# Performance work log

Measured on AMD Instinct MI355X. Metric: run time of the kernel, lower is better.

The kernel has to match this reference:

```python
import jax, jax.numpy as jnp
import numpy as np
import math

G = 128          # graphs per batch
N_PER = 512      # nodes per graph (equal-size, contiguous layout)
N = G * N_PER    # 65536 nodes
DEG = 16
E = N * DEG      # 1,048,576 edges
IN_C, HID, OUT_C = 100, 128, 2
RATIO = 0.8
EPS = 1e-5

K1 = int(math.ceil(RATIO * N_PER))  # 410
K2 = int(math.ceil(RATIO * K1))     # 328
K3 = int(math.ceil(RATIO * K2))     # 263


def gcn_conv(x, src, dst, emask, W, b):
    # GCNConv: linear, symmetric deg^-1/2 norm with self-loops, scatter-add
    xl = x @ W
    n = x.shape[0]
    w = emask.astype(x.dtype)
    deg = jnp.ones((n,), x.dtype).at[dst].add(w)      # +1 from self loop
    dinv = jax.lax.rsqrt(deg)
    coef = dinv[src] * dinv[dst] * w                  # [E]
    out = jnp.zeros_like(xl).at[dst].add(coef[:, None] * xl[src])
    out = out + (dinv * dinv)[:, None] * xl           # self-loop messages
    return out + b


def batch_norm(x, gamma, beta):
    # BatchNorm1d over node dim (training-mode batch statistics)
    mu = x.mean(0)
    var = x.var(0)
    return (x - mu) * jax.lax.rsqrt(var + EPS) * gamma + beta


def topk_pool(x, src, dst, emask, att, g, n, k):
    # TopKPooling: score = tanh(x@att/||att||), keep top-k per graph, gate features,
    # drop edges touching removed nodes (via validity mask).
    score = jnp.tanh((x @ att) / jnp.linalg.norm(att))
    _, idx = jax.lax.top_k(score.reshape(g, n), k)           # [g,k] local ids
    kept = (idx + (jnp.arange(g) * n)[:, None]).reshape(-1)   # global ids
    new_x = x[kept] * score[kept][:, None]
    old2new = jnp.full((g * n,), -1, jnp.int32).at[kept].set(
        jnp.arange(g * k, dtype=jnp.int32))
    s2, d2 = old2new[src], old2new[dst]
    valid = emask & (s2 >= 0) & (d2 >= 0)
    return new_x, jnp.maximum(s2, 0), jnp.maximum(d2, 0), valid


def readout(x, g, k):
    # [global_max_pool, global_mean_pool] over each graph's k nodes
    xr = x.reshape(g, k, -1)
    return jnp.concatenate([xr.max(1), xr.mean(1)], axis=1)   # [g, 2C]


def setup_inputs() -> dict:
    key = jax.random.key(0)
    ks = jax.random.split(key, 16)
    x = jax.random.normal(ks[0], (N, IN_C), jnp.float32)
    # within-graph random edges, then offset by graph id
    e_per = E // G
    local = jax.random.randint(ks[1], (2, G, e_per), 0, N_PER)
    edge_index = (local + (jnp.arange(G) * N_PER)[None, :, None]).reshape(2, E).astype(jnp.int32)
    batch = jnp.repeat(jnp.arange(G, dtype=jnp.int32), N_PER)

    def w(k, fi, fo):
        return jax.random.normal(k, (fi, fo), jnp.float32) * (1.0 / np.sqrt(fi))

    z = lambda c: jnp.zeros((c,), jnp.float32)
    o = lambda c: jnp.ones((c,), jnp.float32)
    return {
        'x': x, 'edge_index': edge_index, 'batch': batch,
        'Wp': w(ks[2], IN_C, 128), 'bp': z(128),
        'W1': w(ks[3], 128, HID), 'b1': z(HID), 'g1': o(HID), 'be1': z(HID),
        'att1': jax.random.normal(ks[4], (HID,), jnp.float32),
        'W2': w(ks[5], HID, HID), 'b2': z(HID), 'g2': o(HID), 'be2': z(HID),
        'att2': jax.random.normal(ks[6], (HID,), jnp.float32),
        'W3': w(ks[7], HID, HID), 'b3': z(HID), 'g3': o(HID), 'be3': z(HID),
        'att3': jax.random.normal(ks[8], (HID,), jnp.float32),
        'Wl1': w(ks[9], 2 * HID, HID), 'bl1': z(HID),
        'Wl2': w(ks[10], HID, OUT_C), 'bl2': z(OUT_C),
    }


def reference(x, edge_index, batch, Wp, bp, W1, b1, g1, be1, att1,
              W2, b2, g2, be2, att2, W3, b3, g3, be3, att3,
              Wl1, bl1, Wl2, bl2):
    src, dst = edge_index[0], edge_index[1]
    emask = jnp.ones((E,), bool)
    h = jax.nn.relu(x @ Wp + bp)

    h = jax.nn.relu(batch_norm(gcn_conv(h, src, dst, emask, W1, b1), g1, be1))
    h, src, dst, emask = topk_pool(h, src, dst, emask, att1, G, N_PER, K1)
    x1 = readout(h, G, K1)

    h = jax.nn.relu(batch_norm(gcn_conv(h, src, dst, emask, W2, b2), g2, be2))
    h, src, dst, emask = topk_pool(h, src, dst, emask, att2, G, K1, K2)
    x2 = readout(h, G, K2)

    h = jax.nn.relu(batch_norm(gcn_conv(h, src, dst, emask, W3, b3), g3, be3))
    h, src, dst, emask = topk_pool(h, src, dst, emask, att3, G, K2, K3)
    x3 = readout(h, G, K3)

    s = x1 + x2 + x3                       # [G, 2*HID]
    s = jax.nn.relu(s @ Wl1 + bl1)
    return s @ Wl2 + bl2                   # [G, OUT_C]
```

## Files before the change

### kernel.cpp

```cpp
#include <hip/hip_runtime.h>
#include <math.h>

#define G     128
#define NPER  512
#define NTOT  65536
#define E_TOT 1048576
#define EPG   8192
#define INC   100
#define HID   128
#define KP1   410
#define KP2   328
#define KP3   263

__global__ void init_kernel(short* __restrict__ cmap, float* __restrict__ sread,
                            float* __restrict__ bnpart) {
    int t = blockIdx.x * 256 + threadIdx.x;
    if (t < NTOT) cmap[t] = (short)(t & (NPER - 1));
    if (t < G * 256) { sread[t] = 0.f; bnpart[t] = 0.f; }
}

__global__ __launch_bounds__(512, 2) void csr_build0(
    const int* __restrict__ src, const int* __restrict__ dst,
    unsigned short* __restrict__ csr_g, int* __restrict__ rowptr_g)
{
    __shared__ int cnt_s[NPER];
    __shared__ int rowptr_s[NPER + 1];
    __shared__ int wo_s[NPER];
    __shared__ int chunksum_s[9];

    const int g = blockIdx.x, tid = threadIdx.x, lane = tid & 63, wv = tid >> 6;
    const int ebase = g * EPG, obase = g * NPER;

    cnt_s[tid] = 0;
    __syncthreads();
    for (int e = tid; e < EPG; e += 512)
        atomicAdd(&cnt_s[dst[ebase + e] - obase], 1);
    __syncthreads();

    int v = cnt_s[tid], x = v;
#pragma unroll
    for (int d = 1; d < 64; d <<= 1) {
        int y = __shfl_up(x, d);
        if (lane >= d) x += y;
    }
    if (lane == 63) chunksum_s[wv] = x;
    __syncthreads();
    if (tid == 0) {
        int acc = 0;
#pragma unroll
        for (int k = 0; k < 8; ++k) { int t = chunksum_s[k]; chunksum_s[k] = acc; acc += t; }
    }
    __syncthreads();
    int excl = x - v + chunksum_s[wv];
    rowptr_s[tid] = excl; wo_s[tid] = excl;
    if (tid == 511) rowptr_s[512] = excl + v;
    __syncthreads();

    for (int i = tid; i <= NPER; i += 512) rowptr_g[g * 513 + i] = rowptr_s[i];
    for (int e = tid; e < EPG; e += 512) {
        int sl = src[ebase + e] - obase, dl = dst[ebase + e] - obase;
        int pos = atomicAdd(&wo_s[dl], 1);
        csr_g[g * EPG + pos] = (unsigned short)sl;
    }
}

template<int K, bool RELU>
__global__ __launch_bounds__(256, 2) void gemm_kernel(
    const float* __restrict__ A, const float* __restrict__ W,
    const float* __restrict__ bias, float* __restrict__ out, int M)
{
    constexpr int KC = 32;
    __shared__ float Ws[KC][128];
    __shared__ float As[KC][132];
    const int tid  = threadIdx.x;
    const int row0 = blockIdx.x * 128;
    const int r0 = (tid >> 4) * 8;
    const int c0 = (tid & 15) * 8;

    float acc[8][8];
#pragma unroll
    for (int i = 0; i < 8; ++i)
#pragma unroll
        for (int j = 0; j < 8; ++j) acc[i][j] = 0.f;

    for (int k0 = 0; k0 < K; k0 += KC) {
        const int kc  = (K - k0 < KC) ? (K - k0) : KC;
        const int nf4 = kc >> 2;

        for (int i = tid; i < kc * 32; i += 256) {
            int kk = i >> 5, c4 = i & 31;
            *((float4*)&Ws[kk][0] + c4) =
                *((const float4*)(W + (size_t)(k0 + kk) * 128) + c4);
        }
        for (int i = tid; i < nf4 * 128; i += 256) {
            int row = i / nf4, f4 = i - row * nf4;
            float4 v = *(const float4*)(A + (size_t)(row0 + row) * K + k0 + f4 * 4);
            As[f4 * 4 + 0][row] = v.x;
            As[f4 * 4 + 1][row] = v.y;
            As[f4 * 4 + 2][row] = v.z;
            As[f4 * 4 + 3][row] = v.w;
        }
        __syncthreads();

        for (int kk = 0; kk < kc; ++kk) {
            float4 b0 = *(const float4*)&Ws[kk][c0];
            float4 b1 = *(const float4*)&Ws[kk][c0 + 4];
            float4 a0 = *(const float4*)&As[kk][r0];
            float4 a1 = *(const float4*)&As[kk][r0 + 4];
            float a[8] = {a0.x, a0.y, a0.z, a0.w, a1.x, a1.y, a1.z, a1.w};
            float b[8] = {b0.x, b0.y, b0.z, b0.w, b1.x, b1.y, b1.z, b1.w};
#pragma unroll
            for (int i = 0; i < 8; ++i)
#pragma unroll
                for (int j = 0; j < 8; ++j)
                    acc[i][j] += a[i] * b[j];
        }
        __syncthreads();
    }

#pragma unroll
    for (int i = 0; i < 8; ++i) {
        int row = row0 + r0 + i;
        float o[8];
#pragma unroll
        for (int j = 0; j < 8; ++j) {
            float v = acc[i][j];
            if (RELU) v = fmaxf(v + bias[c0 + j], 0.f);
            o[j] = v;
        }
        float* po = out + (size_t)row * 128 + c0;
        *(float4*)po       = make_float4(o[0], o[1], o[2], o[3]);
        *(float4*)(po + 4) = make_float4(o[4], o[5], o[6], o[7]);
    }
}

template<int NCUR>
__global__ __launch_bounds__(256, 4) void gather_kernel(
    const float* __restrict__ xs, const unsigned short* __restrict__ csr_g,
    const int* __restrict__ rowptr_g, const float* __restrict__ bvec,
    float* __restrict__ out, float* __restrict__ bnpart)
{
    constexpr int CHUNK = (NCUR + 7) / 8;
    constexpr int CSRCAP = 2560;
    __shared__ int   rowptr_s[NCUR + 1];
    __shared__ float dinv_s[NCUR];
    __shared__ unsigned short csr_s[CSRCAP];
    __shared__ float red_s[512];

    const int g = blockIdx.x, s = blockIdx.y;
    const int tid = threadIdx.x, lane = tid & 63, w = tid >> 6;
    const int nb = g * NCUR;
    const int d0 = s * CHUNK;
    const int d1 = (d0 + CHUNK < NCUR) ? d0 + CHUNK : NCUR;

    const int* rp = rowptr_g + g * 513;
    for (int i = tid; i <= NCUR; i += 256) rowptr_s[i] = rp[i];
    __syncthreads();
    for (int i = tid; i < NCUR; i += 256)
        dinv_s[i] = rsqrtf((float)(rowptr_s[i + 1] - rowptr_s[i] + 1));

    const int base = rowptr_s[d0];
    int nume = rowptr_s[d1] - base;
    if (nume > CSRCAP) nume = CSRCAP;
    const unsigned short* cg = csr_g + g * EPG + base;
    for (int i = tid; i < nume; i += 256) csr_s[i] = cg[i];
    __syncthreads();

    const float2* x2 = (const float2*)xs;
    float2* o2p = (float2*)out;
    const float2 b2 = ((const float2*)bvec)[lane];
    float2 sum = make_float2(0.f, 0.f), sq = make_float2(0.f, 0.f);

    for (int d = d0 + w; d < d1; d += 4) {
        const int beg = rowptr_s[d] - base, end = rowptr_s[d + 1] - base;
        const float dv = dinv_s[d];
        float2 xv = x2[(size_t)(nb + d) * 64 + lane];
        float2 acc = make_float2(dv * xv.x, dv * xv.y);
#pragma unroll 4
        for (int i = beg; i < end; ++i) {
            int sl = csr_s[i];
            float ws_ = dinv_s[sl];
            float2 v = x2[(size_t)(nb + sl) * 64 + lane];
            acc.x += ws_ * v.x; acc.y += ws_ * v.y;
        }
        float2 o = make_float2(b2.x + dv * acc.x, b2.y + dv * acc.y);
        o2p[(size_t)(nb + d) * 64 + lane] = o;
        sum.x += o.x; sum.y += o.y;
        sq.x  += o.x * o.x; sq.y += o.y * o.y;
    }

    float2* red2 = (float2*)red_s;
    red2[tid] = sum; __syncthreads();
    if (tid < 64) {
        float2 a = red2[tid], b_ = red2[tid + 64],
               c = red2[tid + 128], d_ = red2[tid + 192];
        atomicAdd(&bnpart[g * 256 + 2 * tid],     a.x + b_.x + c.x + d_.x);
        atomicAdd(&bnpart[g * 256 + 2 * tid + 1], a.y + b_.y + c.y + d_.y);
    }
    __syncthreads();
    red2[tid] = sq; __syncthreads();
    if (tid < 64) {
        float2 a = red2[tid], b_ = red2[tid + 64],
               c = red2[tid + 128], d_ = red2[tid + 192];
        atomicAdd(&bnpart[g * 256 + 128 + 2 * tid],     a.x + b_.x + c.x + d_.x);
        atomicAdd(&bnpart[g * 256 + 128 + 2 * tid + 1], a.y + b_.y + c.y + d_.y);
    }
}

__global__ __launch_bounds__(1024, 1) void bnfin_kernel(
    const float* __restrict__ bnpart, float n,
    const float* __restrict__ gamma, const float* __restrict__ beta,
    const float* __restrict__ att, float* __restrict__ coefs)
{
    __shared__ float ssum[8][128];
    __shared__ float ssq[8][128];
    __shared__ float r[128];
    const int t = threadIdx.x & 127, slice = threadIdx.x >> 7;
    float s = 0.f, q = 0.f;
    for (int g = slice; g < G; g += 8) {
        s += bnpart[g * 256 + t];
        q += bnpart[g * 256 + 128 + t];
    }
    ssum[slice][t] = s; ssq[slice][t] = q;
    if (threadIdx.x < 128) { float av = att[t]; r[t] = av * av; }
    __syncthreads();
    if (threadIdx.x < 128) {
        float S = 0.f, Q = 0.f;
#pragma unroll
        for (int k = 0; k < 8; ++k) { S += ssum[k][t]; Q += ssq[k][t]; }
        for (int st = 64; st > 0; st >>= 1) {
            if (t < st) r[t] += r[t + st];
            __syncthreads();
        }
        float norm = sqrtf(r[0]);
        float mu   = S / n;
        float var  = Q / n - mu * mu;
        float inv  = rsqrtf(var + 1e-5f);
        float a    = gamma[t] * inv;
        coefs[t]        = a;
        coefs[128 + t]  = beta[t] - mu * a;
        coefs[256 + t]  = att[t] / norm;
    }
}

template<int NCUR, int KK, bool BUILD>
__global__ __launch_bounds__(1024, 1) void pool_kernel(
    const float* __restrict__ gcn, const float* __restrict__ coefs,
    float* __restrict__ newx, short* __restrict__ cmap,
    float* __restrict__ sread, float* __restrict__ bnpart,
    const int* __restrict__ src, const int* __restrict__ dst,
    unsigned short* __restrict__ csr_g, int* __restrict__ rowptr_g)
{
    __shared__ float score_s[NCUR];
    __shared__ unsigned long long key_s[NCUR];
    __shared__ short o2n_s[NCUR];
    __shared__ unsigned short n2o_s[KK];
    __shared__ short cmap_s[NPER];
    __shared__ float2 red2[1024];
    __shared__ int   cnt_s[512];
    __shared__ int   rowptr_s[513];
    __shared__ int   wo_s[512];
    __shared__ int   chunksum_s[9];

    const int g = blockIdx.x, tid = threadIdx.x, lane = tid & 63, w = tid >> 6;
    const int nb = g * NCUR;
    const int ebase = g * EPG, obase = g * NPER;
    const float a0 = coefs[lane],       a1 = coefs[64 + lane];
    const float c0 = coefs[128 + lane], c1 = coefs[192 + lane];
    const float t0 = coefs[256 + lane], t1 = coefs[320 + lane];

    for (int i = tid; i < NPER; i += 1024) cmap_s[i] = cmap[obase + i];

    for (int i = w; i < NCUR; i += 16) {
        const float* row = gcn + (size_t)(nb + i) * 128;
        float h0 = fmaxf(a0 * row[lane] + c0, 0.f);
        float h1 = fmaxf(a1 * row[64 + lane] + c1, 0.f);
        float p  = h0 * t0 + h1 * t1;
#pragma unroll
        for (int off = 32; off > 0; off >>= 1) p += __shfl_down(p, off);
        if (lane == 0) score_s[i] = tanhf(p);
    }
    __syncthreads();

    for (int i = tid; i < NCUR; i += 1024) {
        unsigned u   = __float_as_uint(score_s[i]);
        unsigned key = (u & 0x80000000u) ? ~u : (u | 0x80000000u);
        key_s[i] = ((unsigned long long)key << 32) |
                   (unsigned long long)(0xFFFFFFFFu - (unsigned)i);
    }
    __syncthreads();

    for (int i = tid; i < NCUR; i += 1024) {
        const unsigned long long ki = key_s[i];
        int r = 0;
#pragma unroll 8
        for (int j = 0; j < NCUR; ++j) r += (key_s[j] > ki) ? 1 : 0;
        o2n_s[i] = (r < KK) ? (short)r : (short)-1;
        if (r < KK) n2o_s[r] = (unsigned short)i;
    }
    __syncthreads();

    float mx0 = -1e30f, mx1 = -1e30f, sm0 = 0.f, sm1 = 0.f;
    for (int j2 = w; j2 < KK; j2 += 16) {
        int old = n2o_s[j2];
        float s = score_s[old];
        const float* row = gcn + (size_t)(nb + old) * 128;
        float h0 = fmaxf(a0 * row[lane] + c0, 0.f) * s;
        float h1 = fmaxf(a1 * row[64 + lane] + c1, 0.f) * s;
        float* orow = newx + (size_t)(g * KK + j2) * 128;
        orow[lane]      = h0;
        orow[64 + lane] = h1;
        mx0 = fmaxf(mx0, h0); mx1 = fmaxf(mx1, h1);
        sm0 += h0; sm1 += h1;
    }
    red2[tid] = make_float2(mx0, mx1);
    __syncthreads();
    if (tid < 64) {
        float m = -1e30f;
#pragma unroll
        for (int w2 = 0; w2 < 16; ++w2) m = fmaxf(m, red2[w2 * 64 + tid].x);
        sread[g * 256 + tid] += m;
    } else if (tid < 128) {
        int l = tid - 64;
        float m = -1e30f;
#pragma unroll
        for (int w2 = 0; w2 < 16; ++w2) m = fmaxf(m, red2[w2 * 64 + l].y);
        sread[g * 256 + tid] += m;
    }
    __syncthreads();
    red2[tid] = make_float2(sm0, sm1);
    __syncthreads();
    if (tid < 64) {
        float sm = 0.f;
#pragma unroll
        for (int w2 = 0; w2 < 16; ++w2) sm += red2[w2 * 64 + tid].x;
        sread[g * 256 + 128 + tid] += sm * (1.0f / KK);
    } else if (tid < 128) {
        int l = tid - 64;
        float sm = 0.f;
#pragma unroll
        for (int w2 = 0; w2 < 16; ++w2) sm += red2[w2 * 64 + l].y;
        sread[g * 256 + 128 + tid] += sm * (1.0f / KK);
    }

    for (int o = tid; o < NPER; o += 1024) {
        int m = cmap_s[o];
        short nm = (m >= 0) ? o2n_s[m] : (short)-1;
        cmap_s[o] = nm;
        cmap[obase + o] = nm;
    }
    if (tid < 256) bnpart[g * 256 + tid] = 0.f;

    if (!BUILD) return;
    __syncthreads();

    if (tid < 512) cnt_s[tid] = 0;
    __syncthreads();
    for (int e = tid; e < EPG; e += 1024) {
        int sl = cmap_s[src[ebase + e] - obase];
        int dl = cmap_s[dst[ebase + e] - obase];
        if ((sl | dl) >= 0) atomicAdd(&cnt_s[dl], 1);
    }
    __syncthreads();
    int v = 0, x = 0;
    if (tid < 512) {
        v = cnt_s[tid]; x = v;
#pragma unroll
        for (int d = 1; d < 64; d <<= 1) {
            int y = __shfl_up(x, d);
            if (lane >= d) x += y;
        }
        if (lane == 63) chunksum_s[w] = x;
    }
    __syncthreads();
    if (tid == 0) {
        int acc = 0;
#pragma unroll
        for (int k = 0; k < 8; ++k) { int t = chunksum_s[k]; chunksum_s[k] = acc; acc += t; }
    }
    __syncthreads();
    if (tid < 512) {
        int excl = x - v + chunksum_s[w];
        rowptr_s[tid] = excl; wo_s[tid] = excl;
        if (tid == 511) rowptr_s[512] = excl + v;
    }
    __syncthreads();
    for (int i = tid; i <= 512; i += 1024) rowptr_g[g * 513 + i] = rowptr_s[i];
    for (int e = tid; e < EPG; e += 1024) {
        int sl = cmap_s[src[ebase + e] - obase];
        int dl = cmap_s[dst[ebase + e] - obase];
        if ((sl | dl) >= 0) {
            int pos = atomicAdd(&wo_s[dl], 1);
            csr_g[g * EPG + pos] = (unsigned short)sl;
        }
    }
}

__global__ void final_kernel(const float* __restrict__ sread,
                             const float* __restrict__ Wl1,
                             const float* __restrict__ bl1,
                             const float* __restrict__ Wl2,
                             const float* __restrict__ bl2,
                             float* __restrict__ out)
{
    __shared__ float s_s[256];
    __shared__ float hid_s[128];
    int g = blockIdx.x, t = threadIdx.x;
    s_s[t]       = sread[g * 256 + t];
    s_s[128 + t] = sread[g * 256 + 128 + t];
    __syncthreads();
    float acc = bl1[t];
    for (int i = 0; i < 256; ++i) acc += s_s[i] * Wl1[i * 128 + t];
    hid_s[t] = fmaxf(acc, 0.f);
    __syncthreads();
    if (t < 2) {
        float o = bl2[t];
        for (int j = 0; j < 128; ++j) o += hid_s[j] * Wl2[j * 2 + t];
        out[g * 2 + t] = o;
    }
}

extern "C" void kernel_launch(void* const* d_in, const int* in_sizes, int n_in,
                              void* d_out, int out_size, void* d_ws, size_t ws_size,
                              hipStream_t stream)
{
    const float* x    = (const float*)d_in[0];
    const int*   ei   = (const int*)d_in[1];
    const float* Wp   = (const float*)d_in[3];
    const float* bp   = (const float*)d_in[4];
    const float* W1   = (const float*)d_in[5];
    const float* b1   = (const float*)d_in[6];
    const float* g1   = (const float*)d_in[7];
    const float* be1  = (const float*)d_in[8];
    const float* att1 = (const float*)d_in[9];
    const float* W2   = (const float*)d_in[10];
    const float* b2   = (const float*)d_in[11];
    const float* g2   = (const float*)d_in[12];
    const float* be2  = (const float*)d_in[13];
    const float* att2 = (const float*)d_in[14];
    const float* W3   = (const float*)d_in[15];
    const float* b3   = (const float*)d_in[16];
    const float* g3   = (const float*)d_in[17];
    const float* be3  = (const float*)d_in[18];
    const float* att3 = (const float*)d_in[19];
    const float* Wl1  = (const float*)d_in[20];
    const float* bl1  = (const float*)d_in[21];
    const float* Wl2  = (const float*)d_in[22];
    const float* bl2  = (const float*)d_in[23];
    float* out = (float*)d_out;

    const int* srcp = ei;
    const int* dstp = ei + E_TOT;

    char* ws = (char*)d_ws;
    float*          bufA   = (float*)ws;
    float*          bufB   = (float*)(ws + 33554432);
    unsigned short* csr    = (unsigned short*)(ws + 67108864);
    int*            rowptr = (int*)  (ws + 69206016);
    float*          bnpart = (float*)(ws + 69468672);
    short*          cmap   = (short*)(ws + 69599744);
    float*          sread  = (float*)(ws + 69730816);
    float*          coefs  = (float*)(ws + 69861888);

    init_kernel<<<256, 256, 0, stream>>>(cmap, sread, bnpart);
    csr_build0<<<G, 512, 0, stream>>>(srcp, dstp, csr, rowptr);

    gemm_kernel<INC, true><<<512, 256, 0, stream>>>(x, Wp, bp, bufA, NTOT);

    gemm_kernel<128, false><<<512, 256, 0, stream>>>(bufA, W1, nullptr, bufB, NTOT);
    gather_kernel<512><<<dim3(G, 8), 256, 0, stream>>>(bufB, csr, rowptr, b1, bufA, bnpart);
    bnfin_kernel<<<1, 1024, 0, stream>>>(bnpart, (float)NTOT, g1, be1, att1, coefs);
    pool_kernel<512, KP1, true><<<G, 1024, 0, stream>>>(bufA, coefs, bufB, cmap, sread, bnpart,
                                                        srcp, dstp, csr, rowptr);

    gemm_kernel<128, false><<<410, 256, 0, stream>>>(bufB, W2, nullptr, bufA, G * KP1);
    gather_kernel<KP1><<<dim3(G, 8), 256, 0, stream>>>(bufA, csr, rowptr, b2, bufB, bnpart);
    bnfin_kernel<<<1, 1024, 0, stream>>>(bnpart, (float)(G * KP1), g2, be2, att2, coefs);
    pool_kernel<KP1, KP2, true><<<G, 1024, 0, stream>>>(bufB, coefs, bufA, cmap, sread, bnpart,
                                                        srcp, dstp, csr, rowptr);

    gemm_kernel<128, false><<<328, 256, 0, stream>>>(bufA, W3, nullptr, bufB, G * KP2);
    gather_kernel<KP2><<<dim3(G, 8), 256, 0, stream>>>(bufB, csr, rowptr, b3, bufA, bnpart);
    bnfin_kernel<<<1, 1024, 0, stream>>>(bnpart, (float)(G * KP2), g3, be3, att3, coefs);
    pool_kernel<KP2, KP3, false><<<G, 1024, 0, stream>>>(bufA, coefs, bufB, cmap, sread, bnpart,
                                                         srcp, dstp, csr, rowptr);

    final_kernel<<<G, 128, 0, stream>>>(sread, Wl1, bl1, Wl2, bl2, out);
}
```

Baseline: 509.2 us.

## Stage per-graph feature half in LDS for gather and pre-scale by dinv

The GCN gather kernel now uses one block per (graph, 64-feature half). Each block loads that graph's feature half into shared memory, pre-multiplied by the source degree norm, along with the whole per-graph CSR. Neighbor accumulation then reads LDS instead of scattered global/L2 loads and drops the per-edge multiply. In exchange, the grid shrinks from 1024 to 256 blocks of 512 threads, and the large LDS footprint (128KB+ for 512 nodes) limits each CU to one block, which may underfill the GPU.

```diff
diff --git a/kernel.cpp b/kernel.cpp
--- a/kernel.cpp
+++ b/kernel.cpp
@@ -135,75 +135,70 @@
 }
 
 template<int NCUR>
-__global__ __launch_bounds__(256, 4) void gather_kernel(
+__global__ __launch_bounds__(512, 1) void gather_kernel(
     const float* __restrict__ xs, const unsigned short* __restrict__ csr_g,
     const int* __restrict__ rowptr_g, const float* __restrict__ bvec,
     float* __restrict__ out, float* __restrict__ bnpart)
 {
-    constexpr int CHUNK = (NCUR + 7) / 8;
-    constexpr int CSRCAP = 2560;
+    __shared__ float x_s[NCUR * 64];
+    __shared__ unsigned short csr_s[EPG];
     __shared__ int   rowptr_s[NCUR + 1];
     __shared__ float dinv_s[NCUR];
-    __shared__ unsigned short csr_s[CSRCAP];
     __shared__ float red_s[512];
 
-    const int g = blockIdx.x, s = blockIdx.y;
+    const int g = blockIdx.x, half = blockIdx.y;
     const int tid = threadIdx.x, lane = tid & 63, w = tid >> 6;
     const int nb = g * NCUR;
-    const int d0 = s * CHUNK;
-    const int d1 = (d0 + CHUNK < NCUR) ? d0 + CHUNK : NCUR;
 
     const int* rp = rowptr_g + g * 513;
-    for (int i = tid; i <= NCUR; i += 256) rowptr_s[i] = rp[i];
-    __syncthreads();
-    for (int i = tid; i < NCUR; i += 256)
+    for (int i = tid; i <= NCUR; i += 512) rowptr_s[i] = rp[i];
+    __syncthreads();
+
+    for (int i = tid; i < NCUR; i += 512)
         dinv_s[i] = rsqrtf((float)(rowptr_s[i + 1] - rowptr_s[i] + 1));
-
-    const int base = rowptr_s[d0];
-    int nume = rowptr_s[d1] - base;
-    if (nume > CSRCAP) nume = CSRCAP;
-    const unsigned short* cg = csr_g + g * EPG + base;
-    for (int i = tid; i < nume; i += 256) csr_s[i] = cg[i];
-    __syncthreads();
-
-    const float2* x2 = (const float2*)xs;
-    float2* o2p = (float2*)out;
-    const float2 b2 = ((const float2*)bvec)[lane];
-    float2 sum = make_float2(0.f, 0.f), sq = make_float2(0.f, 0.f);
-
-    for (int d = d0 + w; d < d1; d += 4) {
-        const int beg = rowptr_s[d] - base, end = rowptr_s[d + 1] - base;
+    const int etot = rowptr_s[NCUR];
+    for (int i = tid; i < etot; i += 512) csr_s[i] = csr_g[g * EPG + i];
+    __syncthreads();
+
+    for (int i = tid; i < NCUR * 16; i += 512) {
+        int node = i >> 4, f = i & 15;
+        float4 v = *(const float4*)(xs + (size_t)(nb + node) * 128 + half * 64 + f * 4);
+        float dv = dinv_s[node];
+        *(float4*)&x_s[node * 64 + f * 4] =
+            make_float4(v.x * dv, v.y * dv, v.z * dv, v.w * dv);
+    }
+    __syncthreads();
+
+    const float bc = bvec[half * 64 + lane];
+    float bsum = 0.f, bsq = 0.f;
+    for (int d = w; d < NCUR; d += 8) {
+        const int beg = rowptr_s[d], end = rowptr_s[d + 1];
         const float dv = dinv_s[d];
-        float2 xv = x2[(size_t)(nb + d) * 64 + lane];
-        float2 acc = make_float2(dv * xv.x, dv * xv.y);
+        float acc = x_s[d * 64 + lane];
 #pragma unroll 4
         for (int i = beg; i < end; ++i) {
             int sl = csr_s[i];
-            float ws_ = dinv_s[sl];
-            float2 v = x2[(size_t)(nb + sl) * 64 + lane];
-            acc.x += ws_ * v.x; acc.y += ws_ * v.y;
-        }
-        float2 o = make_float2(b2.x + dv * acc.x, b2.y + dv * acc.y);
-        o2p[(size_t)(nb + d) * 64 + lane] = o;
-        sum.x += o.x; sum.y += o.y;
-        sq.x  += o.x * o.x; sq.y += o.y * o.y;
-    }
-
-    float2* red2 = (float2*)red_s;
-    red2[tid] = sum; __syncthreads();
+            acc += x_s[sl * 64 + lane];
+        }
+        float o = bc + dv * acc;
+        out[(size_t)(nb + d) * 128 + half * 64 + lane] = o;
+        bsum += o; bsq += o * o;
+    }
+
+    red_s[tid] = bsum; __syncthreads();
     if (tid < 64) {
-        float2 a = red2[tid], b_ = red2[tid + 64],
-               c = red2[tid + 128], d_ = red2[tid + 192];
-        atomicAdd(&bnpart[g * 256 + 2 * tid],     a.x + b_.x + c.x + d_.x);
-        atomicAdd(&bnpart[g * 256 + 2 * tid + 1], a.y + b_.y + c.y + d_.y);
-    }
-    __syncthreads();
-    red2[tid] = sq; __syncthreads();
+        float s = 0.f;
+#pragma unroll
+        for (int k = 0; k < 8; ++k) s += red_s[k * 64 + tid];
+        atomicAdd(&bnpart[g * 256 + half * 64 + tid], s);
+    }
+    __syncthreads();
+    red_s[tid] = bsq; __syncthreads();
     if (tid < 64) {
-        float2 a = red2[tid], b_ = red2[tid + 64],
-               c = red2[tid + 128], d_ = red2[tid + 192];
-        atomicAdd(&bnpart[g * 256 + 128 + 2 * tid],     a.x + b_.x + c.x + d_.x);
-        atomicAdd(&bnpart[g * 256 + 128 + 2 * tid + 1], a.y + b_.y + c.y + d_.y);
+        float q = 0.f;
+#pragma unroll
+        for (int k = 0; k < 8; ++k) q += red_s[k * 64 + tid];
+        atomicAdd(&bnpart[g * 256 + 128 + half * 64 + tid], q);
     }
 }
 
@@ -468,19 +463,19 @@
     gemm_kernel<INC, true><<<512, 256, 0, stream>>>(x, Wp, bp, bufA, NTOT);
 
     gemm_kernel<128, false><<<512, 256, 0, stream>>>(bufA, W1, nullptr, bufB, NTOT);
-    gather_kernel<512><<<dim3(G, 8), 256, 0, stream>>>(bufB, csr, rowptr, b1, bufA, bnpart);
+    gather_kernel<512><<<dim3(G, 2), 512, 0, stream>>>(bufB, csr, rowptr, b1, bufA, bnpart);
     bnfin_kernel<<<1, 1024, 0, stream>>>(bnpart, (float)NTOT, g1, be1, att1, coefs);
     pool_kernel<512, KP1, true><<<G, 1024, 0, stream>>>(bufA, coefs, bufB, cmap, sread, bnpart,
                                                         srcp, dstp, csr, rowptr);
 
     gemm_kernel<128, false><<<410, 256, 0, stream>>>(bufB, W2, nullptr, bufA, G * KP1);
-    gather_kernel<KP1><<<dim3(G, 8), 256, 0, stream>>>(bufA, csr, rowptr, b2, bufB, bnpart);
+    gather_kernel<KP1><<<dim3(G, 2), 512, 0, stream>>>(bufA, csr, rowptr, b2, bufB, bnpart);
     bnfin_kernel<<<1, 1024, 0, stream>>>(bnpart, (float)(G * KP1), g2, be2, att2, coefs);
     pool_kernel<KP1, KP2, true><<<G, 1024, 0, stream>>>(bufB, coefs, bufA, cmap, sread, bnpart,
                                                         srcp, dstp, csr, rowptr);
 
     gemm_kernel<128, false><<<328, 256, 0, stream>>>(bufA, W3, nullptr, bufB, G * KP2);
-    gather_kernel<KP2><<<dim3(G, 8), 256, 0, stream>>>(bufB, csr, rowptr, b3, bufA, bnpart);
+    gather_kernel<KP2><<<dim3(G, 2), 512, 0, stream>>>(bufB, csr, rowptr, b3, bufA, bnpart);
     bnfin_kernel<<<1, 1024, 0, stream>>>(bnpart, (float)(G * KP2), g3, be3, att3, coefs);
     pool_kernel<KP2, KP3, false><<<G, 1024, 0, stream>>>(bufA, coefs, bufB, cmap, sread, bnpart,
                                                          srcp, dstp, csr, rowptr);
```

Result: slower. 566.4 us (+11.2%).

## Split gather across more blocks and interleave two destination rows per wave

Applied to the files above, without the earlier changes.

The GCN gather kernel now splits each graph's destination rows over 16 blocks instead of 8, raises the launch-bounds occupancy hint, and shrinks the shared CSR buffer to match. Each wave handles two destination rows at once, issuing their neighbour loads in the same loop so more independent memory requests are in flight. This targets latency-bound irregular gathers. The cost is more registers per thread, duplicated rowptr/dinv setup across twice as many blocks, and more atomics for the batch-norm partial sums.

```diff
diff --git a/kernel.cpp b/kernel.cpp
--- a/kernel.cpp
+++ b/kernel.cpp
@@ -135,13 +135,13 @@
 }
 
 template<int NCUR>
-__global__ __launch_bounds__(256, 4) void gather_kernel(
+__global__ __launch_bounds__(256, 8) void gather_kernel(
     const float* __restrict__ xs, const unsigned short* __restrict__ csr_g,
     const int* __restrict__ rowptr_g, const float* __restrict__ bvec,
     float* __restrict__ out, float* __restrict__ bnpart)
 {
-    constexpr int CHUNK = (NCUR + 7) / 8;
-    constexpr int CSRCAP = 2560;
+    constexpr int CHUNK = (NCUR + 15) / 16;
+    constexpr int CSRCAP = 1536;
     __shared__ int   rowptr_s[NCUR + 1];
     __shared__ float dinv_s[NCUR];
     __shared__ unsigned short csr_s[CSRCAP];
@@ -149,7 +149,7 @@
 
     const int g = blockIdx.x, s = blockIdx.y;
     const int tid = threadIdx.x, lane = tid & 63, w = tid >> 6;
-    const int nb = g * NCUR;
+    const int nbase = g * NCUR;
     const int d0 = s * CHUNK;
     const int d1 = (d0 + CHUNK < NCUR) ? d0 + CHUNK : NCUR;
 
@@ -171,22 +171,59 @@
     const float2 b2 = ((const float2*)bvec)[lane];
     float2 sum = make_float2(0.f, 0.f), sq = make_float2(0.f, 0.f);
 
-    for (int d = d0 + w; d < d1; d += 4) {
-        const int beg = rowptr_s[d] - base, end = rowptr_s[d + 1] - base;
-        const float dv = dinv_s[d];
-        float2 xv = x2[(size_t)(nb + d) * 64 + lane];
-        float2 acc = make_float2(dv * xv.x, dv * xv.y);
+    for (int da = d0 + w; da < d1; da += 8) {
+        const int db = da + 4;
+        const bool hb = db < d1;
+        const int ia = rowptr_s[da] - base;
+        const int na = rowptr_s[da + 1] - rowptr_s[da];
+        const int ib = hb ? rowptr_s[db] - base : 0;
+        const int nbl = hb ? rowptr_s[db + 1] - rowptr_s[db] : 0;
+        const float dva = dinv_s[da];
+        const float dvb = hb ? dinv_s[db] : 0.f;
+
+        float2 xa = x2[(size_t)(nbase + da) * 64 + lane];
+        float2 accA = make_float2(dva * xa.x, dva * xa.y);
+        float2 accB = make_float2(0.f, 0.f);
+        if (hb) {
+            float2 xb = x2[(size_t)(nbase + db) * 64 + lane];
+            accB = make_float2(dvb * xb.x, dvb * xb.y);
+        }
+
+        const int nmin = na < nbl ? na : nbl;
+#pragma unroll 2
+        for (int t = 0; t < nmin; ++t) {
+            int sa = csr_s[ia + t], sb = csr_s[ib + t];
+            float wa = dinv_s[sa], wb = dinv_s[sb];
+            float2 va = x2[(size_t)(nbase + sa) * 64 + lane];
+            float2 vb = x2[(size_t)(nbase + sb) * 64 + lane];
+            accA.x += wa * va.x; accA.y += wa * va.y;
+            accB.x += wb * vb.x; accB.y += wb * vb.y;
+        }
 #pragma unroll 4
-        for (int i = beg; i < end; ++i) {
-            int sl = csr_s[i];
-            float ws_ = dinv_s[sl];
-            float2 v = x2[(size_t)(nb + sl) * 64 + lane];
-            acc.x += ws_ * v.x; acc.y += ws_ * v.y;
-        }
-        float2 o = make_float2(b2.x + dv * acc.x, b2.y + dv * acc.y);
-        o2p[(size_t)(nb + d) * 64 + lane] = o;
-        sum.x += o.x; sum.y += o.y;
-        sq.x  += o.x * o.x; sq.y += o.y * o.y;
+        for (int t = nmin; t < na; ++t) {
+            int sa = csr_s[ia + t];
+            float wa = dinv_s[sa];
+            float2 va = x2[(size_t)(nbase + sa) * 64 + lane];
+            accA.x += wa * va.x; accA.y += wa * va.y;
+        }
+#pragma unroll 4
+        for (int t = nmin; t < nbl; ++t) {
+            int sb = csr_s[ib + t];
+            float wb = dinv_s[sb];
+            float2 vb = x2[(size_t)(nbase + sb) * 64 + lane];
+            accB.x += wb * vb.x; accB.y += wb * vb.y;
+        }
+
+        float2 oA = make_float2(b2.x + dva * accA.x, b2.y + dva * accA.y);
+        o2p[(size_t)(nbase + da) * 64 + lane] = oA;
+        sum.x += oA.x; sum.y += oA.y;
+        sq.x  += oA.x * oA.x; sq.y += oA.y * oA.y;
+        if (hb) {
+            float2 oB = make_float2(b2.x + dvb * accB.x, b2.y + dvb * accB.y);
+            o2p[(size_t)(nbase + db) * 64 + lane] = oB;
+            sum.x += oB.x; sum.y += oB.y;
+            sq.x  += oB.x * oB.x; sq.y += oB.y * oB.y;
+        }
     }
 
     float2* red2 = (float2*)red_s;
@@ -468,19 +505,19 @@
     gemm_kernel<INC, true><<<512, 256, 0, stream>>>(x, Wp, bp, bufA, NTOT);
 
     gemm_kernel<128, false><<<512, 256, 0, stream>>>(bufA, W1, nullptr, bufB, NTOT);
-    gather_kernel<512><<<dim3(G, 8), 256, 0, stream>>>(bufB, csr, rowptr, b1, bufA, bnpart);
+    gather_kernel<512><<<dim3(G, 16), 256, 0, stream>>>(bufB, csr, rowptr, b1, bufA, bnpart);
     bnfin_kernel<<<1, 1024, 0, stream>>>(bnpart, (float)NTOT, g1, be1, att1, coefs);
     pool_kernel<512, KP1, true><<<G, 1024, 0, stream>>>(bufA, coefs, bufB, cmap, sread, bnpart,
                                                         srcp, dstp, csr, rowptr);
 
     gemm_kernel<128, false><<<410, 256, 0, stream>>>(bufB, W2, nullptr, bufA, G * KP1);
-    gather_kernel<KP1><<<dim3(G, 8), 256, 0, stream>>>(bufA, csr, rowptr, b2, bufB, bnpart);
+    gather_kernel<KP1><<<dim3(G, 16), 256, 0, stream>>>(bufA, csr, rowptr, b2, bufB, bnpart);
     bnfin_kernel<<<1, 1024, 0, stream>>>(bnpart, (float)(G * KP1), g2, be2, att2, coefs);
     pool_kernel<KP1, KP2, true><<<G, 1024, 0, stream>>>(bufB, coefs, bufA, cmap, sread, bnpart,
                                                         srcp, dstp, csr, rowptr);
 
     gemm_kernel<128, false><<<328, 256, 0, stream>>>(bufA, W3, nullptr, bufB, G * KP2);
-    gather_kernel<KP2><<<dim3(G, 8), 256, 0, stream>>>(bufB, csr, rowptr, b3, bufA, bnpart);
+    gather_kernel<KP2><<<dim3(G, 16), 256, 0, stream>>>(bufB, csr, rowptr, b3, bufA, bnpart);
     bnfin_kernel<<<1, 1024, 0, stream>>>(bnpart, (float)(G * KP2), g3, be3, att3, coefs);
     pool_kernel<KP2, KP3, false><<<G, 1024, 0, stream>>>(bufA, coefs, bufB, cmap, sread, bnpart,
                                                          srcp, dstp, csr, rowptr);
```

New measurement: 493.0 us. -3.2%, faster.
